# Performance work log

Measured on AMD Instinct MI355X. Metric: run time of the kernel, lower is better.

Reference implementation:

```python
import jax, jax.numpy as jnp
import numpy as np

B, L, K, H = 512, 512, 103, 512
I = K + 2  # LSTM input = obs(103) + fed-back pos(2)


def setup_inputs() -> dict:
    key = jax.random.key(0)
    ks = jax.random.split(key, 14)
    s = 0.02
    return {
        "x": jax.random.normal(ks[0], (B, L, K), dtype=jnp.float32),
        "pos": jax.random.normal(ks[1], (B, L, 2), dtype=jnp.float32),
        "hidden_state": jnp.zeros((B, H), dtype=jnp.float32),
        "cell_state": jnp.zeros((B, H), dtype=jnp.float32),
        # LSTM params (PyTorch layout: gates ordered i,f,g,o)
        "W_ih": jax.random.normal(ks[2], (4 * H, I), dtype=jnp.float32) * s,
        "W_hh": jax.random.normal(ks[3], (4 * H, H), dtype=jnp.float32) * s,
        "b_ih": jnp.zeros((4 * H,), dtype=jnp.float32),
        "b_hh": jnp.zeros((4 * H,), dtype=jnp.float32),
        # MLP: H -> 64 -> 16 -> 2, all ReLU
        "W1": jax.random.normal(ks[4], (64, H), dtype=jnp.float32) * s,
        "b1": jnp.zeros((64,), dtype=jnp.float32),
        "W2": jax.random.normal(ks[5], (16, 64), dtype=jnp.float32) * s,
        "b2": jnp.zeros((16,), dtype=jnp.float32),
        "W3": jax.random.normal(ks[6], (2, 16), dtype=jnp.float32) * s,
        "b3": jnp.zeros((2,), dtype=jnp.float32),
    }


def reference(x, pos, hidden_state, cell_state, W_ih, W_hh, b_ih, b_hh,
              W1, b1, W2, b2, W3, b3):
    b = b_ih + b_hh

    def step(carry, x_t):
        h, c, ip = carry  # (B,H),(B,H),(B,2)
        inp = jnp.concatenate([x_t, ip], axis=-1)  # (B, I)
        gates = inp @ W_ih.T + h @ W_hh.T + b      # (B, 4H)
        i, f, g, o = jnp.split(gates, 4, axis=-1)
        c = jax.nn.sigmoid(f) * c + jax.nn.sigmoid(i) * jnp.tanh(g)
        h = jax.nn.sigmoid(o) * jnp.tanh(c)
        y = jax.nn.relu(h @ W1.T + b1)
        y = jax.nn.relu(y @ W2.T + b2)
        y = jax.nn.relu(y @ W3.T + b3)  # (B,2) predicted next pos
        return (h, c, y), y

    xs = jnp.swapaxes(x, 0, 1)  # (L,B,K)
    (h, c, _), ys = jax.lax.scan(step, (hidden_state, cell_state, pos[:, 0, :]), xs)
    predicted_pos = jnp.swapaxes(ys, 0, 1)  # (B,L,2)
    return predicted_pos, h, c
```

## Files before the change

### kernel.cpp

```cpp
#include <hip/hip_runtime.h>

#define NB 512
#define NL 512
#define NK 103
#define NH 512
#define NI 105
#define XROW (NL * NK)

typedef _Float16 half8 __attribute__((ext_vector_type(8)));
typedef _Float16 half4 __attribute__((ext_vector_type(4)));
typedef float floatx4 __attribute__((ext_vector_type(4)));

#define XB_STR 136
#define B2_STR 136
#define YST_STR 72
#define Y2_STR 16
#define OFF_XB 0
#define OFF_B2 34816
#define OFF_YST 52224
#define OFF_Y2 61440
#define OFF_FR 63488
#define SMEM_BYTES 65280

#define SPIN_MAX (1 << 20)

#define A_LOAD(p)  __hip_atomic_load((p),  __ATOMIC_RELAXED, __HIP_MEMORY_SCOPE_AGENT)
#define A_STORE(p, v) __hip_atomic_store((p), (v), __ATOMIC_RELAXED, __HIP_MEMORY_SCOPE_AGENT)

__device__ __forceinline__ float fast_sigmoid(float v) {
  v = fminf(fmaxf(v, -30.f), 30.f);
  return __builtin_amdgcn_rcpf(1.f + __expf(-v));
}
__device__ __forceinline__ float fast_tanh(float v) {
  v = fminf(fmaxf(v, -15.f), 15.f);
  float e = __expf(-2.f * v);
  return (1.f - e) * __builtin_amdgcn_rcpf(1.f + e);
}

__global__ void __launch_bounds__(256, 1)
lstm_persist(const float* __restrict__ x, const float* __restrict__ pos,
             const float* __restrict__ h0, const float* __restrict__ c0,
             const float* __restrict__ Wih, const float* __restrict__ Whh,
             const float* __restrict__ bih, const float* __restrict__ bhh,
             const float* __restrict__ W1, const float* __restrict__ b1,
             const float* __restrict__ W2, const float* __restrict__ b2,
             const float* __restrict__ W3, const float* __restrict__ b3,
             float* __restrict__ out, void* __restrict__ ws)
{
  extern __shared__ char smem[];
  _Float16* XB  = (_Float16*)(smem + OFF_XB);
  _Float16* B2s = (_Float16*)(smem + OFF_B2);
  _Float16* YST = (_Float16*)(smem + OFF_YST);
  _Float16* Y2  = (_Float16*)(smem + OFF_Y2);
  _Float16* HTX = Y2;
  float* FR  = (float*)(smem + OFF_FR);
  float* b1s = FR;
  float* b2s = FR + 64;
  float* w3s = FR + 80;
  float* b3s = FR + 112;
  float* wy0 = FR + 114;
  float* wy1 = FR + 178;
  float* bgs = FR + 242;
  float* ypres = FR + 306;
  volatile int* abflag = (volatile int*)(FR + 440);

  const int tid = threadIdx.x;
  const int g  = blockIdx.x >> 5;
  const int cs = blockIdx.x & 31;
  const int w  = tid >> 6, l = tid & 63;
  const int c16 = l & 15, q = l >> 4;
  const int rh = w >> 1;
  const int ch = w & 1;

  unsigned* flags = (unsigned*)ws;
  _Float16* hbuf = (_Float16*)((char*)ws + 4096);
  const int HBUF = NB * NH;

  if (tid == 0) *abflag = 0;
  {
    unsigned* xz = (unsigned*)XB;
    for (int i = tid; i < 8704; i += 256) xz[i] = 0;
  }
  for (int idx = tid; idx < 64 * 128; idx += 256) {
    int cc = idx >> 7, k = idx & 127;
    int gr = (cc >> 4) * NH + cs * 16 + (cc & 15);
    float v = (k < NK) ? Wih[(size_t)gr * NI + k] : 0.f;
    B2s[cc * B2_STR + k] = (_Float16)v;
  }
  if (tid < 64) {
    int gr = (tid >> 4) * NH + cs * 16 + (tid & 15);
    wy0[tid] = Wih[(size_t)gr * NI + 103];
    wy1[tid] = Wih[(size_t)gr * NI + 104];
    bgs[tid] = bih[gr] + bhh[gr];
    b1s[tid] = b1[tid];
  }
  if (tid < 16) b2s[tid] = b2[tid];
  if (tid < 32) w3s[tid] = W3[tid];
  if (tid < 2)  b3s[tid] = b3[tid];

  {
    int row = tid >> 2, cc = tid & 3;
    const float* src = h0 + (size_t)(64 * g + row) * NH + cs * 16 + cc * 4;
    union { unsigned long long u; half4 h; } cv;
    cv.h[0] = (_Float16)src[0]; cv.h[1] = (_Float16)src[1];
    cv.h[2] = (_Float16)src[2]; cv.h[3] = (_Float16)src[3];
    A_STORE((unsigned long long*)(hbuf + (size_t)cs * 8192 + (size_t)(64 * g + row) * 16 + cc * 4), cv.u);
  }

  half8 bfr[4][16];
  #pragma unroll
  for (int ct = 0; ct < 4; ++ct) {
    const int rown = ch ? (ct * 16 + c16) : (ct * NH + cs * 16 + c16);
    const float* rp = (ch ? W1 : Whh) + (size_t)rown * NH;
    #pragma unroll
    for (int kk = 0; kk < 16; ++kk) {
      const float* p = rp + kk * 32 + q * 8;
      floatx4 f0 = *(const floatx4*)(p);
      floatx4 f1 = *(const floatx4*)(p + 4);
      half8 hv;
      hv[0]=(_Float16)f0[0]; hv[1]=(_Float16)f0[1]; hv[2]=(_Float16)f0[2]; hv[3]=(_Float16)f0[3];
      hv[4]=(_Float16)f1[0]; hv[5]=(_Float16)f1[1]; hv[6]=(_Float16)f1[2]; hv[7]=(_Float16)f1[3];
      bfr[ct][kk] = hv;
    }
  }
  half8 w2f[2];
  if (ch) {
    #pragma unroll
    for (int kk = 0; kk < 2; ++kk) {
      const float* p = W2 + c16 * 64 + kk * 32 + q * 8;
      floatx4 f0 = *(const floatx4*)(p);
      floatx4 f1 = *(const floatx4*)(p + 4);
      half8 hv;
      hv[0]=(_Float16)f0[0]; hv[1]=(_Float16)f0[1]; hv[2]=(_Float16)f0[2]; hv[3]=(_Float16)f0[3];
      hv[4]=(_Float16)f1[0]; hv[5]=(_Float16)f1[1]; hv[6]=(_Float16)f1[2]; hv[7]=(_Float16)f1[3];
      w2f[kk] = hv;
    }
  }
  float cacc[2][4];
  if (!ch) {
    #pragma unroll
    for (int rt = 0; rt < 2; ++rt)
      #pragma unroll
      for (int reg = 0; reg < 4; ++reg)
        cacc[rt][reg] = c0[(size_t)(64 * g + 32 * rh + 16 * rt + q * 4 + reg) * NH + cs * 16 + c16];
  }

  auto xstage = [&](int t1) {
    _Float16* xb = XB + (size_t)(t1 & 1) * 64 * XB_STR;
    const int row = 32 * rh + (l >> 1);
    const int p = l & 1;
    const float* src = x + (size_t)(64 * g + row) * XROW + (size_t)t1 * NK + p * 52;
    _Float16* dst = xb + row * XB_STR + p * 52;
    const int nfull = p ? 12 : 13;
    for (int cnk = 0; cnk < nfull; ++cnk) {
      float f0 = src[cnk * 4 + 0], f1 = src[cnk * 4 + 1];
      float f2 = src[cnk * 4 + 2], f3 = src[cnk * 4 + 3];
      half4 hv; hv[0]=(_Float16)f0; hv[1]=(_Float16)f1; hv[2]=(_Float16)f2; hv[3]=(_Float16)f3;
      *(half4*)(dst + cnk * 4) = hv;
    }
    if (p) {
      dst[48] = (_Float16)src[48];
      dst[49] = (_Float16)src[49];
      dst[50] = (_Float16)src[50];
    }
  };

  unsigned ep = 1;
  auto gbar = [&](void) {
    __syncthreads();
    if (w == 0) {
      if (l == 0)
        A_STORE(flags + ((g << 5) + cs) * 4, ep);
      unsigned* f = flags + ((g << 5) + (l & 31)) * 4;
      int spins = 0;
      while (A_LOAD(f) < ep) {
        __builtin_amdgcn_s_sleep(1);
        if (++spins > SPIN_MAX) { *abflag = 1; break; }
      }
    }
    __syncthreads();
    asm volatile("" ::: "memory");
    ep++;
  };

  __syncthreads();
  if (!ch) xstage(0);
  gbar();
  if (*abflag) return;

  for (int t = 0; t <= NL; ++t) {
    const _Float16* hr = hbuf + (size_t)(t & 1) * HBUF;

    floatx4 acc[4][2] = {};
    const int growb = 64 * g + 32 * rh + c16;
    #pragma unroll
    for (int kc = 0; kc < 2; ++kc) {
      half8 ar[2][8];
      #pragma unroll
      for (int kk = 0; kk < 8; ++kk) {
        #pragma unroll
        for (int rt = 0; rt < 2; ++rt) {
          const _Float16* ap = hr + (size_t)((kc * 8 + kk) * 2 + (q >> 1)) * 8192
                               + (size_t)(growb + 16 * rt) * 16 + (q & 1) * 8;
          const unsigned long long* up = (const unsigned long long*)ap;
          union { unsigned long long u[2]; half8 h; } cv;
          cv.u[0] = A_LOAD(up);
          cv.u[1] = A_LOAD(up + 1);
          ar[rt][kk] = cv.h;
        }
      }
      #pragma unroll
      for (int kk = 0; kk < 8; ++kk)
        #pragma unroll
        for (int ct = 0; ct < 4; ++ct)
          #pragma unroll
          for (int rt = 0; rt < 2; ++rt)
            acc[ct][rt] = __builtin_amdgcn_mfma_f32_16x16x32_f16(
                ar[rt][kk], bfr[ct][kc * 8 + kk], acc[ct][rt], 0, 0, 0);
    }

    if (!ch && t < NL) {
      const _Float16* xb = XB + (size_t)(t & 1) * 64 * XB_STR;
      #pragma unroll
      for (int kb = 0; kb < 4; ++kb) {
        half8 ax[2];
        #pragma unroll
        for (int rt = 0; rt < 2; ++rt)
          ax[rt] = *(const half8*)(xb + (32 * rh + 16 * rt + c16) * XB_STR + kb * 32 + q * 8);
        #pragma unroll
        for (int ct = 0; ct < 4; ++ct) {
          half8 bf = *(const half8*)(B2s + (ct * 16 + c16) * B2_STR + kb * 32 + q * 8);
          #pragma unroll
          for (int rt = 0; rt < 2; ++rt)
            acc[ct][rt] = __builtin_amdgcn_mfma_f32_16x16x32_f16(ax[rt], bf, acc[ct][rt], 0, 0, 0);
        }
      }
      if (t + 1 < NL) xstage(t + 1);
    }

    if (ch) {
      if (t == 0) {
        if (l < 32) {
          int row = 32 * rh + l;
          const float* pp = pos + (size_t)(64 * g + row) * (NL * 2);
          ypres[row * 2 + 0] = pp[0];
          ypres[row * 2 + 1] = pp[1];
        }
      } else {
        #pragma unroll
        for (int ct = 0; ct < 4; ++ct)
          #pragma unroll
          for (int rt = 0; rt < 2; ++rt)
            #pragma unroll
            for (int reg = 0; reg < 4; ++reg) {
              int row = 32 * rh + 16 * rt + q * 4 + reg;
              float v = acc[ct][rt][reg] + b1s[ct * 16 + c16];
              YST[row * YST_STR + ct * 16 + c16] = (_Float16)fmaxf(v, 0.f);
            }
        floatx4 a2c[2] = {};
        #pragma unroll
        for (int kk2 = 0; kk2 < 2; ++kk2)
          #pragma unroll
          for (int rt = 0; rt < 2; ++rt) {
            half8 af = *(const half8*)(YST + (32 * rh + 16 * rt + c16) * YST_STR + kk2 * 32 + q * 8);
            a2c[rt] = __builtin_amdgcn_mfma_f32_16x16x32_f16(af, w2f[kk2], a2c[rt], 0, 0, 0);
          }
        #pragma unroll
        for (int rt = 0; rt < 2; ++rt)
          #pragma unroll
          for (int reg = 0; reg < 4; ++reg) {
            int row = 32 * rh + 16 * rt + q * 4 + reg;
            float v = a2c[rt][reg] + b2s[c16];
            Y2[row * Y2_STR + c16] = (_Float16)fmaxf(v, 0.f);
          }
        if (l < 32) {
          int row = 32 * rh + l;
          float y0 = b3s[0], y1 = b3s[1];
          #pragma unroll
          for (int k = 0; k < 16; ++k) {
            float vv = (float)Y2[row * Y2_STR + k];
            y0 += vv * w3s[k];
            y1 += vv * w3s[16 + k];
          }
          y0 = fmaxf(y0, 0.f); y1 = fmaxf(y1, 0.f);
          ypres[row * 2 + 0] = y0;
          ypres[row * 2 + 1] = y1;
          if (cs == 0) {
            float2* op = (float2*)(out + (size_t)(64 * g + row) * (NL * 2) + (size_t)(t - 1) * 2);
            *op = make_float2(y0, y1);
          }
        }
      }
    }
    __syncthreads();

    if (!ch && t < NL) {
      #pragma unroll
      for (int rt = 0; rt < 2; ++rt)
        #pragma unroll
        for (int reg = 0; reg < 4; ++reg) {
          int rl = 32 * rh + 16 * rt + q * 4 + reg;
          float yp0 = ypres[rl * 2], yp1 = ypres[rl * 2 + 1];
          float gi = acc[0][rt][reg] + bgs[c16]      + yp0 * wy0[c16]      + yp1 * wy1[c16];
          float gf = acc[1][rt][reg] + bgs[16 + c16] + yp0 * wy0[16 + c16] + yp1 * wy1[16 + c16];
          float gg = acc[2][rt][reg] + bgs[32 + c16] + yp0 * wy0[32 + c16] + yp1 * wy1[32 + c16];
          float go = acc[3][rt][reg] + bgs[48 + c16] + yp0 * wy0[48 + c16] + yp1 * wy1[48 + c16];
          float iv = fast_sigmoid(gi);
          float fv = fast_sigmoid(gf);
          float gv = fast_tanh(gg);
          float ov = fast_sigmoid(go);
          float cn = fv * cacc[rt][reg] + iv * gv;
          cacc[rt][reg] = cn;
          float hn = ov * fast_tanh(cn);
          HTX[rl * 16 + c16] = (_Float16)hn;
          if (t == NL - 1) {
            out[(size_t)(NB * NL * 2) + (size_t)(64 * g + rl) * NH + cs * 16 + c16] = hn;
            out[(size_t)(NB * NL * 2) + (size_t)(NB * NH) + (size_t)(64 * g + rl) * NH + cs * 16 + c16] = cn;
          }
        }
    }

    if (t < NL) {
      __syncthreads();
      {
        const int row = tid >> 2, cc = tid & 3;
        unsigned long long v = *(const unsigned long long*)(HTX + row * 16 + cc * 4);
        _Float16* hw = hbuf + (size_t)((t + 1) & 1) * HBUF;
        A_STORE((unsigned long long*)(hw + (size_t)cs * 8192
                                      + (size_t)(64 * g + row) * 16 + cc * 4), v);
      }
      gbar();
      if (*abflag) return;
    }
  }
}

extern "C" void kernel_launch(void* const* d_in, const int* in_sizes, int n_in,
                              void* d_out, int out_size, void* d_ws, size_t ws_size,
                              hipStream_t stream) {
  (void)in_sizes; (void)n_in; (void)out_size; (void)ws_size;
  const float* x   = (const float*)d_in[0];
  const float* pos = (const float*)d_in[1];
  const float* h0  = (const float*)d_in[2];
  const float* c0  = (const float*)d_in[3];
  const float* Wih = (const float*)d_in[4];
  const float* Whh = (const float*)d_in[5];
  const float* bih = (const float*)d_in[6];
  const float* bhh = (const float*)d_in[7];
  const float* W1  = (const float*)d_in[8];
  const float* b1  = (const float*)d_in[9];
  const float* W2  = (const float*)d_in[10];
  const float* b2  = (const float*)d_in[11];
  const float* W3  = (const float*)d_in[12];
  const float* b3  = (const float*)d_in[13];
  float* out = (float*)d_out;

  hipMemsetAsync(d_ws, 0, 4096, stream);

  void* args[] = { (void*)&x, (void*)&pos, (void*)&h0, (void*)&c0,
                   (void*)&Wih, (void*)&Whh, (void*)&bih, (void*)&bhh,
                   (void*)&W1, (void*)&b1, (void*)&W2, (void*)&b2,
                   (void*)&W3, (void*)&b3, (void*)&out, (void*)&d_ws };

  hipError_t err = hipLaunchCooperativeKernel(
      reinterpret_cast<void*>(lstm_persist),
      dim3(256, 1, 1), dim3(256, 1, 1), args, (unsigned)SMEM_BYTES, stream);
  if (err != hipSuccess) {
    (void)hipGetLastError();
    lstm_persist<<<dim3(256, 1, 1), dim3(256, 1, 1), SMEM_BYTES, stream>>>(
        x, pos, h0, c0, Wih, Whh, bih, bhh, W1, b1, W2, b2, W3, b3, out, d_ws);
  }
}
```

Measured before the change: 6.215 ms.

## Stage the group's hidden-state slice into LDS after per-slice flag waits

Each block now waits on each peer slice's flag with its own thread and cooperatively copies its group's 64-row hidden-state slice from global memory into a padded LDS buffer. The MFMA recurrent matmul then reads A fragments from LDS instead of issuing many scattered atomic global loads per wave. The intent is to replace redundant global traffic with one coalesced copy, and to fold the barrier wait into that copy. In exchange LDS use roughly doubles to about 128 KB, which needs the dynamic shared memory attribute raised, and an extra block-wide sync is added each step.

```diff
diff --git a/kernel.cpp b/kernel.cpp
--- a/kernel.cpp
+++ b/kernel.cpp
@@ -10,22 +10,28 @@
 typedef _Float16 half8 __attribute__((ext_vector_type(8)));
 typedef _Float16 half4 __attribute__((ext_vector_type(4)));
 typedef float floatx4 __attribute__((ext_vector_type(4)));
-
+typedef int int4v __attribute__((ext_vector_type(4)));
+
+union U16 { int4v i; half8 h; unsigned long long u[2]; };
+
+#define H_SSTR 2064
 #define XB_STR 136
 #define B2_STR 136
 #define YST_STR 72
 #define Y2_STR 16
-#define OFF_XB 0
-#define OFF_B2 34816
-#define OFF_YST 52224
-#define OFF_Y2 61440
-#define OFF_FR 63488
-#define SMEM_BYTES 65280
+#define OFF_H   0
+#define OFF_XB  66048
+#define OFF_B2  100864
+#define OFF_YST 118272
+#define OFF_Y2  127488
+#define OFF_FR  129536
+#define SMEM_BYTES 131328
 
 #define SPIN_MAX (1 << 20)
 
 #define A_LOAD(p)  __hip_atomic_load((p),  __ATOMIC_RELAXED, __HIP_MEMORY_SCOPE_AGENT)
 #define A_STORE(p, v) __hip_atomic_store((p), (v), __ATOMIC_RELAXED, __HIP_MEMORY_SCOPE_AGENT)
+
 
 __device__ __forceinline__ float fast_sigmoid(float v) {
   v = fminf(fmaxf(v, -30.f), 30.f);
@@ -48,7 +54,6 @@
              float* __restrict__ out, void* __restrict__ ws)
 {
   extern __shared__ char smem[];
-  _Float16* XB  = (_Float16*)(smem + OFF_XB);
   _Float16* B2s = (_Float16*)(smem + OFF_B2);
   _Float16* YST = (_Float16*)(smem + OFF_YST);
   _Float16* Y2  = (_Float16*)(smem + OFF_Y2);
@@ -73,12 +78,11 @@
   const int ch = w & 1;
 
   unsigned* flags = (unsigned*)ws;
-  _Float16* hbuf = (_Float16*)((char*)ws + 4096);
-  const int HBUF = NB * NH;
+  char* hbase = (char*)ws + 4096;
 
   if (tid == 0) *abflag = 0;
   {
-    unsigned* xz = (unsigned*)XB;
+    unsigned* xz = (unsigned*)(smem + OFF_XB);
     for (int i = tid; i < 8704; i += 256) xz[i] = 0;
   }
   for (int idx = tid; idx < 64 * 128; idx += 256) {
@@ -99,12 +103,13 @@
   if (tid < 2)  b3s[tid] = b3[tid];
 
   {
-    int row = tid >> 2, cc = tid & 3;
-    const float* src = h0 + (size_t)(64 * g + row) * NH + cs * 16 + cc * 4;
+    const int r = tid >> 2, hb = tid & 3;
+    const float* src = h0 + (size_t)(64 * g + r) * NH + cs * 16 + hb * 4;
     union { unsigned long long u; half4 h; } cv;
     cv.h[0] = (_Float16)src[0]; cv.h[1] = (_Float16)src[1];
     cv.h[2] = (_Float16)src[2]; cv.h[3] = (_Float16)src[3];
-    A_STORE((unsigned long long*)(hbuf + (size_t)cs * 8192 + (size_t)(64 * g + row) * 16 + cc * 4), cv.u);
+    A_STORE((unsigned long long*)(hbase + (size_t)cs * 16384
+                                  + (size_t)(64 * g + r) * 32 + hb * 8), cv.u);
   }
 
   half8 bfr[4][16];
@@ -146,7 +151,7 @@
   }
 
   auto xstage = [&](int t1) {
-    _Float16* xb = XB + (size_t)(t1 & 1) * 64 * XB_STR;
+    _Float16* xb = (_Float16*)(smem + OFF_XB) + (size_t)(t1 & 1) * 64 * XB_STR;
     const int row = 32 * rh + (l >> 1);
     const int p = l & 1;
     const float* src = x + (size_t)(64 * g + row) * XROW + (size_t)t1 * NK + p * 52;
@@ -165,62 +170,69 @@
     }
   };
 
-  unsigned ep = 1;
-  auto gbar = [&](void) {
-    __syncthreads();
-    if (w == 0) {
-      if (l == 0)
-        A_STORE(flags + ((g << 5) + cs) * 4, ep);
-      unsigned* f = flags + ((g << 5) + (l & 31)) * 4;
+  auto fpub = [&](unsigned val) {
+    if (tid == 0) A_STORE(flags + ((g << 5) + cs) * 4, val);
+  };
+
+  auto hstage = [&](int par, unsigned need) {
+    const int s = tid & 31, rb = tid >> 5;
+    {
+      unsigned* f = flags + ((g << 5) + s) * 4;
       int spins = 0;
-      while (A_LOAD(f) < ep) {
+      while (A_LOAD(f) < need) {
         __builtin_amdgcn_s_sleep(1);
         if (++spins > SPIN_MAX) { *abflag = 1; break; }
       }
     }
-    __syncthreads();
-    asm volatile("" ::: "memory");
-    ep++;
+    const char* gsrc = hbase + (size_t)par * 524288
+                     + (size_t)s * 16384 + (size_t)(64 * g + rb * 8) * 32;
+    char* ldst = smem + OFF_H + s * H_SSTR + rb * 256;
+    unsigned long long v[32];
+    #pragma unroll
+    for (int j = 0; j < 8; ++j) {
+      const unsigned long long* up = (const unsigned long long*)(gsrc + j * 32);
+      v[j*4+0] = A_LOAD(up);     v[j*4+1] = A_LOAD(up + 1);
+      v[j*4+2] = A_LOAD(up + 2); v[j*4+3] = A_LOAD(up + 3);
+    }
+    #pragma unroll
+    for (int j = 0; j < 8; ++j) {
+      U16 a, b;
+      a.u[0] = v[j*4+0]; a.u[1] = v[j*4+1];
+      b.u[0] = v[j*4+2]; b.u[1] = v[j*4+3];
+      *(int4v*)(ldst + j * 32)      = a.i;
+      *(int4v*)(ldst + j * 32 + 16) = b.i;
+    }
   };
 
   __syncthreads();
   if (!ch) xstage(0);
-  gbar();
+  __syncthreads();
+  fpub(1);
+  hstage(0, 1);
+  __syncthreads();
   if (*abflag) return;
 
   for (int t = 0; t <= NL; ++t) {
-    const _Float16* hr = hbuf + (size_t)(t & 1) * HBUF;
 
     floatx4 acc[4][2] = {};
-    const int growb = 64 * g + 32 * rh + c16;
-    #pragma unroll
-    for (int kc = 0; kc < 2; ++kc) {
-      half8 ar[2][8];
+    {
+      const char* base0 = smem + OFF_H + (q >> 1) * H_SSTR
+                        + (32 * rh + c16) * 32 + (q & 1) * 16;
       #pragma unroll
-      for (int kk = 0; kk < 8; ++kk) {
-        #pragma unroll
-        for (int rt = 0; rt < 2; ++rt) {
-          const _Float16* ap = hr + (size_t)((kc * 8 + kk) * 2 + (q >> 1)) * 8192
-                               + (size_t)(growb + 16 * rt) * 16 + (q & 1) * 8;
-          const unsigned long long* up = (const unsigned long long*)ap;
-          union { unsigned long long u[2]; half8 h; } cv;
-          cv.u[0] = A_LOAD(up);
-          cv.u[1] = A_LOAD(up + 1);
-          ar[rt][kk] = cv.h;
-        }
-      }
-      #pragma unroll
-      for (int kk = 0; kk < 8; ++kk)
-        #pragma unroll
-        for (int ct = 0; ct < 4; ++ct)
-          #pragma unroll
-          for (int rt = 0; rt < 2; ++rt)
-            acc[ct][rt] = __builtin_amdgcn_mfma_f32_16x16x32_f16(
-                ar[rt][kk], bfr[ct][kc * 8 + kk], acc[ct][rt], 0, 0, 0);
+      for (int kk = 0; kk < 16; ++kk) {
+        const char* bp = base0 + kk * 2 * H_SSTR;
+        half8 a0 = *(const half8*)(bp);
+        half8 a1 = *(const half8*)(bp + 16 * 32);
+        #pragma unroll
+        for (int ct = 0; ct < 4; ++ct) {
+          acc[ct][0] = __builtin_amdgcn_mfma_f32_16x16x32_f16(a0, bfr[ct][kk], acc[ct][0], 0, 0, 0);
+          acc[ct][1] = __builtin_amdgcn_mfma_f32_16x16x32_f16(a1, bfr[ct][kk], acc[ct][1], 0, 0, 0);
+        }
+      }
     }
 
     if (!ch && t < NL) {
-      const _Float16* xb = XB + (size_t)(t & 1) * 64 * XB_STR;
+      const _Float16* xb = (const _Float16*)(smem + OFF_XB) + (size_t)(t & 1) * 64 * XB_STR;
       #pragma unroll
       for (int kb = 0; kb < 4; ++kb) {
         half8 ax[2];
@@ -323,13 +335,16 @@
     if (t < NL) {
       __syncthreads();
       {
-        const int row = tid >> 2, cc = tid & 3;
-        unsigned long long v = *(const unsigned long long*)(HTX + row * 16 + cc * 4);
-        _Float16* hw = hbuf + (size_t)((t + 1) & 1) * HBUF;
-        A_STORE((unsigned long long*)(hw + (size_t)cs * 8192
-                                      + (size_t)(64 * g + row) * 16 + cc * 4), v);
-      }
-      gbar();
+        const int r = tid >> 2, hb = tid & 3;
+        char* dst = hbase + (size_t)((t + 1) & 1) * 524288
+                  + (size_t)cs * 16384 + (size_t)(64 * g + r) * 32 + hb * 8;
+        unsigned long long v = *(const unsigned long long*)(HTX + r * 16 + hb * 4);
+        A_STORE((unsigned long long*)dst, v);
+      }
+      __syncthreads();
+      fpub((unsigned)(t + 2));
+      hstage((t + 1) & 1, (unsigned)(t + 2));
+      __syncthreads();
       if (*abflag) return;
     }
   }
@@ -357,6 +372,9 @@
 
   hipMemsetAsync(d_ws, 0, 4096, stream);
 
+  hipFuncSetAttribute(reinterpret_cast<const void*>(lstm_persist),
+                      hipFuncAttributeMaxDynamicSharedMemorySize, SMEM_BYTES);
+
   void* args[] = { (void*)&x, (void*)&pos, (void*)&h0, (void*)&c0,
                    (void*)&Wih, (void*)&Whh, (void*)&bih, (void*)&bhh,
                    (void*)&W1, (void*)&b1, (void*)&W2, (void*)&b2,
```

Measured after the change: 8.206 ms. 1.32x slower.
